# Kernel optimization log

Measured on AMD Instinct MI355X. Metric: run time of the kernel, lower is better.

The kernel has to match this reference:

```python
import jax, jax.numpy as jnp
import numpy as np

N = 50000          # nodes
E = 800000         # edges (avg in-degree 16)
IN_FEATS = 256
H = 4              # num_heads
D = 32             # out_feats per head
NEG_SLOPE = 0.2


def setup_inputs() -> dict:
    key = jax.random.key(0)
    k1, k2, k3, k4, k5, k6 = jax.random.split(key, 6)
    feat = jax.random.normal(k1, (N, IN_FEATS), dtype=jnp.float32)
    src = jax.random.randint(k2, (E,), 0, N, dtype=jnp.int32)
    dst = jax.random.randint(k3, (E,), 0, N, dtype=jnp.int32)
    # parameters (xavier-ish scale)
    W = jax.random.normal(k4, (IN_FEATS, H * D), dtype=jnp.float32) * (2.0 / (IN_FEATS + H * D)) ** 0.5
    attn_l = jax.random.normal(k5, (H, D), dtype=jnp.float32) * 0.1
    attn_r = jax.random.normal(k6, (H, D), dtype=jnp.float32) * 0.1
    bias = jnp.zeros((H * D,), dtype=jnp.float32)
    return {"feat": feat, "src": src, "dst": dst, "W": W,
            "attn_l": attn_l, "attn_r": attn_r, "bias": bias}


def reference(feat, src, dst, W, attn_l, attn_r, bias):
    # dense projection: [N, H, D]
    ft = (feat @ W).reshape(N, H, D)
    # per-node attention logits: [N, H]
    el = jnp.einsum('nhd,hd->nh', ft, attn_l)
    er = jnp.einsum('nhd,hd->nh', ft, attn_r)
    # SDDMM u_add_v + leaky relu: per-edge scores [E, H]
    e = jax.nn.leaky_relu(el[src] + er[dst], negative_slope=NEG_SLOPE)
    # edge softmax over incoming edges of each dst node (segment softmax)
    m = jax.ops.segment_max(e, dst, num_segments=N)          # [N, H], -inf for empty
    e_exp = jnp.exp(e - m[dst])                               # [E, H]
    s = jax.ops.segment_sum(e_exp, dst, num_segments=N)       # [N, H]
    a = e_exp / s[dst]                                        # [E, H]
    # SpMM u_mul_e: weighted aggregation to dst nodes
    rst = jax.ops.segment_sum(ft[src] * a[:, :, None], dst, num_segments=N)  # [N, H, D]
    rst = rst + bias.reshape(1, H, D)
    return rst
```

## Files before the change

### kernel.cpp

```cpp
#include <hip/hip_runtime.h>
#include <hip/hip_bf16.h>
#include <math.h>

#define N_NODES 50000
#define N_EDGES 800000
#define IN_F 256
#define HD 128
#define NHEAD 4
#define NB_SCAN 196

typedef __attribute__((ext_vector_type(8))) short bf16x8;
typedef __attribute__((ext_vector_type(4))) float f32x4;

__device__ __forceinline__ float lrelu(float x){ return x > 0.f ? x : 0.2f * x; }

__device__ __forceinline__ unsigned short f32_to_bf16_rn(float x){
    union { float f; unsigned int u; } v; v.f = x;
    unsigned int r = v.u + 0x7FFFu + ((v.u >> 16) & 1u);
    return (unsigned short)(r >> 16);
}
__device__ __forceinline__ float bf16_to_f32(unsigned short h){
    union { unsigned int u; float f; } v; v.u = ((unsigned int)h) << 16;
    return v.f;
}
__device__ __forceinline__ float bflo(unsigned int u){
    union { unsigned int x; float f; } v; v.x = u << 16; return v.f;
}
__device__ __forceinline__ float bfhi(unsigned int u){
    union { unsigned int x; float f; } v; v.x = u & 0xFFFF0000u; return v.f;
}

__global__ void zero_ints(int* __restrict__ p, int n){
    int i = blockIdx.x * blockDim.x + threadIdx.x;
    if (i < n) p[i] = 0;
}

__global__ __launch_bounds__(256) void wsplit_kernel(const float* __restrict__ W,
                                                     unsigned short* __restrict__ Wt_hi,
                                                     unsigned short* __restrict__ Wt_lo){
    int gid = blockIdx.x * 256 + threadIdx.x;
    int n = gid >> 8;
    int k = gid & 255;
    float x = W[(size_t)k * HD + n];
    unsigned short h = f32_to_bf16_rn(x);
    float r = x - bf16_to_f32(h);
    unsigned short l = f32_to_bf16_rn(r);
    Wt_hi[gid] = h;
    Wt_lo[gid] = l;
}

__global__ __launch_bounds__(256) void gemm_kernel(const float* __restrict__ feat,
                                                   const unsigned short* __restrict__ Wt_hi,
                                                   const unsigned short* __restrict__ Wt_lo,
                                                   const float* __restrict__ attn_l,
                                                   const float* __restrict__ attn_r,
                                                   unsigned short* __restrict__ ftb,
                                                   float* __restrict__ el,
                                                   float* __restrict__ er){
    __shared__ unsigned short Ah[128][72];
    __shared__ unsigned short Al[128][72];
    __shared__ unsigned short Bh[128][72];
    __shared__ unsigned short Bl[128][72];

    const int tid  = threadIdx.x;
    const int lane = tid & 63;
    const int wave = tid >> 6;
    const int wrow = wave * 32;
    const int lrow = lane & 15;
    const int lkh  = (lane >> 4) * 8;
    const int row0 = blockIdx.x * 128;

    f32x4 acc[2][8];
#pragma unroll
    for (int i = 0; i < 2; i++)
#pragma unroll
        for (int j = 0; j < 8; j++) acc[i][j] = (f32x4){0.f, 0.f, 0.f, 0.f};

    const int srow = tid >> 1;
    const int skh  = (tid & 1) * 32;

    for (int kc = 0; kc < 4; ++kc){
        const int k0 = kc * 64;
        {
            int gr = row0 + srow;
            const float* fp = feat + (size_t)gr * IN_F + k0 + skh;
            unsigned short* ah = &Ah[srow][skh];
            unsigned short* al = &Al[srow][skh];
#pragma unroll
            for (int u = 0; u < 8; ++u){
                float4 v = make_float4(0.f,0.f,0.f,0.f);
                if (gr < N_NODES) v = *(const float4*)(fp + 4 * u);
                ushort4 h, l;
                h.x = f32_to_bf16_rn(v.x); l.x = f32_to_bf16_rn(v.x - bf16_to_f32(h.x));
                h.y = f32_to_bf16_rn(v.y); l.y = f32_to_bf16_rn(v.y - bf16_to_f32(h.y));
                h.z = f32_to_bf16_rn(v.z); l.z = f32_to_bf16_rn(v.z - bf16_to_f32(h.z));
                h.w = f32_to_bf16_rn(v.w); l.w = f32_to_bf16_rn(v.w - bf16_to_f32(h.w));
                *(ushort4*)(ah + 4 * u) = h;
                *(ushort4*)(al + 4 * u) = l;
            }
        }
        {
            const unsigned short* bh = Wt_hi + srow * 256 + k0 + skh;
            const unsigned short* bl = Wt_lo + srow * 256 + k0 + skh;
#pragma unroll
            for (int u = 0; u < 4; ++u){
                *(uint4*)(&Bh[srow][skh + 8 * u]) = *(const uint4*)(bh + 8 * u);
                *(uint4*)(&Bl[srow][skh + 8 * u]) = *(const uint4*)(bl + 8 * u);
            }
        }
        __syncthreads();
#pragma unroll
        for (int kk = 0; kk < 2; ++kk){
            const int kb = kk * 32 + lkh;
            bf16x8 ah0 = *(const bf16x8*)(&Ah[wrow + lrow][kb]);
            bf16x8 ah1 = *(const bf16x8*)(&Ah[wrow + 16 + lrow][kb]);
            bf16x8 al0 = *(const bf16x8*)(&Al[wrow + lrow][kb]);
            bf16x8 al1 = *(const bf16x8*)(&Al[wrow + 16 + lrow][kb]);
#pragma unroll
            for (int nf = 0; nf < 8; ++nf){
                bf16x8 bh = *(const bf16x8*)(&Bh[nf * 16 + lrow][kb]);
                bf16x8 bl = *(const bf16x8*)(&Bl[nf * 16 + lrow][kb]);
                acc[0][nf] = __builtin_amdgcn_mfma_f32_16x16x32_bf16(ah0, bh, acc[0][nf], 0, 0, 0);
                acc[1][nf] = __builtin_amdgcn_mfma_f32_16x16x32_bf16(ah1, bh, acc[1][nf], 0, 0, 0);
                acc[0][nf] = __builtin_amdgcn_mfma_f32_16x16x32_bf16(ah0, bl, acc[0][nf], 0, 0, 0);
                acc[1][nf] = __builtin_amdgcn_mfma_f32_16x16x32_bf16(ah1, bl, acc[1][nf], 0, 0, 0);
                acc[0][nf] = __builtin_amdgcn_mfma_f32_16x16x32_bf16(al0, bh, acc[0][nf], 0, 0, 0);
                acc[1][nf] = __builtin_amdgcn_mfma_f32_16x16x32_bf16(al1, bh, acc[1][nf], 0, 0, 0);
            }
        }
        __syncthreads();
    }
    float alv[8], arv[8];
#pragma unroll
    for (int nf = 0; nf < 8; ++nf){
        alv[nf] = attn_l[lrow + nf * 16];
        arv[nf] = attn_r[lrow + nf * 16];
    }
#pragma unroll
    for (int mf = 0; mf < 2; ++mf){
#pragma unroll
        for (int r = 0; r < 4; ++r){
            int gr = row0 + wrow + mf * 16 + (lane >> 4) * 4 + r;
            if (gr < N_NODES){
                unsigned short* op = ftb + (size_t)gr * HD + lrow;
#pragma unroll
                for (int nf = 0; nf < 8; ++nf) op[nf * 16] = f32_to_bf16_rn(acc[mf][nf][r]);
            }
            float pl0 = acc[mf][0][r] * alv[0] + acc[mf][1][r] * alv[1];
            float pl1 = acc[mf][2][r] * alv[2] + acc[mf][3][r] * alv[3];
            float pl2 = acc[mf][4][r] * alv[4] + acc[mf][5][r] * alv[5];
            float pl3 = acc[mf][6][r] * alv[6] + acc[mf][7][r] * alv[7];
            float pr0 = acc[mf][0][r] * arv[0] + acc[mf][1][r] * arv[1];
            float pr1 = acc[mf][2][r] * arv[2] + acc[mf][3][r] * arv[3];
            float pr2 = acc[mf][4][r] * arv[4] + acc[mf][5][r] * arv[5];
            float pr3 = acc[mf][6][r] * arv[6] + acc[mf][7][r] * arv[7];
#pragma unroll
            for (int m = 1; m <= 8; m <<= 1){
                pl0 += __shfl_xor(pl0, m, 64); pl1 += __shfl_xor(pl1, m, 64);
                pl2 += __shfl_xor(pl2, m, 64); pl3 += __shfl_xor(pl3, m, 64);
                pr0 += __shfl_xor(pr0, m, 64); pr1 += __shfl_xor(pr1, m, 64);
                pr2 += __shfl_xor(pr2, m, 64); pr3 += __shfl_xor(pr3, m, 64);
            }
            if ((lane & 15) == 0 && gr < N_NODES){
                *(float4*)(el + (size_t)gr * NHEAD) = make_float4(pl0, pl1, pl2, pl3);
                *(float4*)(er + (size_t)gr * NHEAD) = make_float4(pr0, pr1, pr2, pr3);
            }
        }
    }
}

__global__ void degree_kernel(const int* __restrict__ dst, int* __restrict__ deg,
                              int* __restrict__ rank){
    int e = blockIdx.x * blockDim.x + threadIdx.x;
    if (e < N_EDGES) rank[e] = atomicAdd(&deg[dst[e]], 1);
}

__global__ __launch_bounds__(256) void scan_part(const int* __restrict__ deg,
                                                 int* __restrict__ row_off,
                                                 int* __restrict__ blk_sums){
    __shared__ int lds[256];
    int tid = threadIdx.x;
    int i = blockIdx.x * 256 + tid;
    int v = (i < N_NODES) ? deg[i] : 0;
    int x = v;
    lds[tid] = x;
    __syncthreads();
    for (int off = 1; off < 256; off <<= 1){
        int t = (tid >= off) ? lds[tid - off] : 0;
        __syncthreads();
        x += t;
        lds[tid] = x;
        __syncthreads();
    }
    if (i < N_NODES) row_off[i] = x - v;
    if (tid == 255) blk_sums[blockIdx.x] = x;
}

__global__ __launch_bounds__(256) void scan_mid(int* __restrict__ blk_sums,
                                                int* __restrict__ blk_off){
    __shared__ int lds[256];
    int tid = threadIdx.x;
    int v = (tid < NB_SCAN) ? blk_sums[tid] : 0;
    int x = v;
    lds[tid] = x;
    __syncthreads();
    for (int off = 1; off < 256; off <<= 1){
        int t = (tid >= off) ? lds[tid - off] : 0;
        __syncthreads();
        x += t;
        lds[tid] = x;
        __syncthreads();
    }
    blk_off[tid] = x - v;
}

__global__ __launch_bounds__(256) void scan_add(int* __restrict__ row_off,
                                                const int* __restrict__ blk_off){
    int i = blockIdx.x * 256 + threadIdx.x;
    if (i < N_NODES) row_off[i] += blk_off[blockIdx.x];
    if (blockIdx.x == 0 && threadIdx.x == 0) row_off[N_NODES] = N_EDGES;
}

__global__ void scatter_kernel(const int* __restrict__ src, const int* __restrict__ dst,
                               const int* __restrict__ rank, const int* __restrict__ row_off,
                               int* __restrict__ csr_src){
    int e = blockIdx.x * blockDim.x + threadIdx.x;
    if (e >= N_EDGES) return;
    csr_src[row_off[dst[e]] + rank[e]] = src[e];
}

__global__ __launch_bounds__(256) void aggregate_kernel(const unsigned short* __restrict__ ftb,
                                                        const int* __restrict__ csr_src,
                                                        const float* __restrict__ el,
                                                        const float* __restrict__ er,
                                                        const int* __restrict__ row_off,
                                                        const float* __restrict__ bias,
                                                        float* __restrict__ out){
    int n    = blockIdx.x * 4 + (threadIdx.x >> 6);
    int lane = threadIdx.x & 63;
    int h    = lane >> 4;
    int beg  = row_off[n], end = row_off[n + 1];
    float4 ern = *(const float4*)(er + (size_t)n * NHEAD);

    float a0 = 0.f, a1 = 0.f, ws = 0.f;
    for (int base = beg; base < end; base += 64){
        int cnt = end - base; if (cnt > 64) cnt = 64;
        int   s_l = 0;
        float w0l = 0.f, w1l = 0.f, w2l = 0.f, w3l = 0.f;
        if (lane < cnt){
            s_l = csr_src[base + lane];
            float4 elv = *(const float4*)(el + (size_t)s_l * NHEAD);
            w0l = __expf(lrelu(elv.x + ern.x));
            w1l = __expf(lrelu(elv.y + ern.y));
            w2l = __expf(lrelu(elv.z + ern.z));
            w3l = __expf(lrelu(elv.w + ern.w));
        }
#pragma unroll 4
        for (int j = 0; j < cnt; ++j){
            int s = __shfl(s_l, j, 64);
            float w0 = __shfl(w0l, j, 64);
            float w1 = __shfl(w1l, j, 64);
            float w2 = __shfl(w2l, j, 64);
            float w3 = __shfl(w3l, j, 64);
            float w = (h == 0) ? w0 : (h == 1) ? w1 : (h == 2) ? w2 : w3;
            unsigned int f = *(const unsigned int*)(ftb + (size_t)s * HD + 2 * lane);
            a0 += w * bflo(f);
            a1 += w * bfhi(f);
            ws += w;
        }
    }
    float inv = (end > beg) ? 1.f / ws : 0.f;
    float2 o;
    o.x = a0 * inv + bias[2 * lane + 0];
    o.y = a1 * inv + bias[2 * lane + 1];
    *(float2*)(out + (size_t)n * HD + 2 * lane) = o;
}

extern "C" void kernel_launch(void* const* d_in, const int* in_sizes, int n_in,
                              void* d_out, int out_size, void* d_ws, size_t ws_size,
                              hipStream_t stream){
    const float* feat   = (const float*)d_in[0];
    const int*   src    = (const int*)  d_in[1];
    const int*   dst    = (const int*)  d_in[2];
    const float* W      = (const float*)d_in[3];
    const float* attn_l = (const float*)d_in[4];
    const float* attn_r = (const float*)d_in[5];
    const float* bias   = (const float*)d_in[6];
    float* out = (float*)d_out;
    char*  ws  = (char*)d_ws;

    unsigned short* ftb = (unsigned short*)(ws + 0);
    float* el      = (float*)(ws + 12800000);
    float* er      = (float*)(ws + 13600000);
    int*   deg     = (int*)  (ws + 14400000);
    int*   rank    = (int*)  (ws + 14600000);
    int*   row_off = (int*)  (ws + 17800000);
    int*   csr_src = (int*)  (ws + 18000064);

    unsigned short* Wt_hi = (unsigned short*)csr_src;
    unsigned short* Wt_lo = Wt_hi + 32768;
    int* blk_sums = (int*)(((char*)csr_src) + 131072);
    int* blk_off  = blk_sums + 256;

    zero_ints<<<(N_NODES + 255) / 256, 256, 0, stream>>>(deg, N_NODES);
    wsplit_kernel<<<128, 256, 0, stream>>>(W, Wt_hi, Wt_lo);
    gemm_kernel<<<(N_NODES + 127) / 128, 256, 0, stream>>>(feat, Wt_hi, Wt_lo,
                                                           attn_l, attn_r, ftb, el, er);
    degree_kernel<<<(N_EDGES + 255) / 256, 256, 0, stream>>>(dst, deg, rank);
    scan_part<<<NB_SCAN, 256, 0, stream>>>(deg, row_off, blk_sums);
    scan_mid<<<1, 256, 0, stream>>>(blk_sums, blk_off);
    scan_add<<<NB_SCAN, 256, 0, stream>>>(row_off, blk_off);
    scatter_kernel<<<(N_EDGES + 255) / 256, 256, 0, stream>>>(src, dst, rank, row_off, csr_src);
    aggregate_kernel<<<(N_NODES + 3) / 4, 256, 0, stream>>>(ftb, csr_src, el, er,
                                                            row_off, bias, out);
}
```

Baseline: 248.0 us.

## Gather four edges per wave with 16-byte loads and LDS-staged weights

The aggregation kernel now splits each 64-lane wave into four 16-lane groups. Each group processes a different incoming edge, and each lane loads 8 bf16 features with one 16-byte load instead of 2 per edge. Per-edge source indices and attention weights are staged in LDS instead of broadcast with five shuffles per edge. Partial sums from the four groups are combined with xor-shuffles at the end, and only half the lanes write float4 outputs. The aim is more memory-level parallelism and fewer instructions per edge, at the cost of more accumulator registers and a final cross-group reduction.

Result: faster. 225.2 us (-9.2%).

```diff
diff --git a/kernel.cpp b/kernel.cpp
--- a/kernel.cpp
+++ b/kernel.cpp
@@ -236,44 +236,69 @@
                                                         const int* __restrict__ row_off,
                                                         const float* __restrict__ bias,
                                                         float* __restrict__ out){
-    int n    = blockIdx.x * 4 + (threadIdx.x >> 6);
-    int lane = threadIdx.x & 63;
-    int h    = lane >> 4;
-    int beg  = row_off[n], end = row_off[n + 1];
-    float4 ern = *(const float4*)(er + (size_t)n * NHEAD);
-
-    float a0 = 0.f, a1 = 0.f, ws = 0.f;
+    __shared__ float lw[4][64][4];
+    __shared__ int   ls[4][64];
+
+    const int wv   = threadIdx.x >> 6;
+    const int n    = blockIdx.x * 4 + wv;
+    const int lane = threadIdx.x & 63;
+    const int g    = lane >> 4;
+    const int l    = lane & 15;
+    const int h    = l >> 2;
+    const int beg  = row_off[n], end = row_off[n + 1];
+    const float4 ern = *(const float4*)(er + (size_t)n * NHEAD);
+
+    float a[8];
+#pragma unroll
+    for (int k = 0; k < 8; ++k) a[k] = 0.f;
+    float wsum = 0.f;
+
     for (int base = beg; base < end; base += 64){
         int cnt = end - base; if (cnt > 64) cnt = 64;
-        int   s_l = 0;
-        float w0l = 0.f, w1l = 0.f, w2l = 0.f, w3l = 0.f;
+        float4 w4 = make_float4(0.f, 0.f, 0.f, 0.f);
+        int s_l = 0;
         if (lane < cnt){
             s_l = csr_src[base + lane];
             float4 elv = *(const float4*)(el + (size_t)s_l * NHEAD);
-            w0l = __expf(lrelu(elv.x + ern.x));
-            w1l = __expf(lrelu(elv.y + ern.y));
-            w2l = __expf(lrelu(elv.z + ern.z));
-            w3l = __expf(lrelu(elv.w + ern.w));
-        }
-#pragma unroll 4
-        for (int j = 0; j < cnt; ++j){
-            int s = __shfl(s_l, j, 64);
-            float w0 = __shfl(w0l, j, 64);
-            float w1 = __shfl(w1l, j, 64);
-            float w2 = __shfl(w2l, j, 64);
-            float w3 = __shfl(w3l, j, 64);
-            float w = (h == 0) ? w0 : (h == 1) ? w1 : (h == 2) ? w2 : w3;
-            unsigned int f = *(const unsigned int*)(ftb + (size_t)s * HD + 2 * lane);
-            a0 += w * bflo(f);
-            a1 += w * bfhi(f);
-            ws += w;
-        }
-    }
-    float inv = (end > beg) ? 1.f / ws : 0.f;
-    float2 o;
-    o.x = a0 * inv + bias[2 * lane + 0];
-    o.y = a1 * inv + bias[2 * lane + 1];
-    *(float2*)(out + (size_t)n * HD + 2 * lane) = o;
+            w4.x = __expf(lrelu(elv.x + ern.x));
+            w4.y = __expf(lrelu(elv.y + ern.y));
+            w4.z = __expf(lrelu(elv.z + ern.z));
+            w4.w = __expf(lrelu(elv.w + ern.w));
+        }
+        ls[wv][lane] = s_l;
+        *(float4*)(&lw[wv][lane][0]) = w4;
+        asm volatile("s_waitcnt lgkmcnt(0)" ::: "memory");
+        __builtin_amdgcn_sched_barrier(0);
+        for (int j0 = 0; j0 < cnt; j0 += 4){
+            int j = j0 + g;
+            float w = lw[wv][j][h];
+            int   s = ls[wv][j];
+            uint4 f = *(const uint4*)(ftb + (size_t)s * HD + 8 * l);
+            a[0] += w * bflo(f.x); a[1] += w * bfhi(f.x);
+            a[2] += w * bflo(f.y); a[3] += w * bfhi(f.y);
+            a[4] += w * bflo(f.z); a[5] += w * bfhi(f.z);
+            a[6] += w * bflo(f.w); a[7] += w * bfhi(f.w);
+            wsum += w;
+        }
+        __builtin_amdgcn_sched_barrier(0);
+    }
+#pragma unroll
+    for (int m = 16; m <= 32; m <<= 1){
+#pragma unroll
+        for (int k = 0; k < 8; ++k) a[k] += __shfl_xor(a[k], m, 64);
+        wsum += __shfl_xor(wsum, m, 64);
+    }
+    float inv = (end > beg) ? 1.f / wsum : 0.f;
+    if (g < 2){
+        int col = 8 * l + 4 * g;
+        float4 b4 = *(const float4*)(bias + col);
+        float4 o;
+        o.x = a[4 * g + 0] * inv + b4.x;
+        o.y = a[4 * g + 1] * inv + b4.y;
+        o.z = a[4 * g + 2] * inv + b4.z;
+        o.w = a[4 * g + 3] * inv + b4.w;
+        *(float4*)(out + (size_t)n * HD + col) = o;
+    }
 }
 
 extern "C" void kernel_launch(void* const* d_in, const int* in_sizes, int n_in,
```
